# Kernel tuning notes

Measured on AMD Instinct MI355X. Metric: run time of the kernel, lower is better.

Reference implementation:

```python
import jax, jax.numpy as jnp
import numpy as np

N, E, F_IN, H, C = 169343, 1166243, 128, 128, 40
BN_EPS = 1e-5


def setup_inputs() -> dict:
    key = jax.random.key(0)
    ks = jax.random.split(key, 16)
    inp = {
        "x": jax.random.normal(ks[0], (N, F_IN), jnp.float32),
        "edge_index": jax.random.randint(ks[1], (2, E), 0, N, dtype=jnp.int64),
        "W1": jax.random.normal(ks[2], (F_IN, H), jnp.float32) * (1.0 / np.sqrt(F_IN)),
        "b1": jnp.zeros((H,), jnp.float32),
        "g1": jnp.ones((H,), jnp.float32),
        "be1": jnp.zeros((H,), jnp.float32),
        "m1": jax.random.normal(ks[3], (H,), jnp.float32) * 0.1,
        "v1": jax.random.uniform(ks[4], (H,), jnp.float32, 0.5, 1.5),
        "W2": jax.random.normal(ks[5], (H, H), jnp.float32) * (1.0 / np.sqrt(H)),
        "b2": jnp.zeros((H,), jnp.float32),
        "g2": jnp.ones((H,), jnp.float32),
        "be2": jnp.zeros((H,), jnp.float32),
        "m2": jax.random.normal(ks[6], (H,), jnp.float32) * 0.1,
        "v2": jax.random.uniform(ks[7], (H,), jnp.float32, 0.5, 1.5),
        "W3": jax.random.normal(ks[8], (H, C), jnp.float32) * (1.0 / np.sqrt(H)),
        "b3": jnp.zeros((C,), jnp.float32),
    }
    return inp


def _gcn_conv(h, W, b, src, dst, norm, n_nodes):
    # GCNConv: out = D^-1/2 (A+I) D^-1/2 (h W) + b
    hw = h @ W                                   # [N, H] dense GEMM
    msgs = hw[src] * norm[:, None]               # [E', H] gather (irregular)
    agg = jax.ops.segment_sum(msgs, dst, num_segments=n_nodes)  # scatter-add
    return agg + b


def _bn_eval(h, gamma, beta, mean, var):
    return (h - mean) * jax.lax.rsqrt(var + BN_EPS) * gamma + beta


def reference(x, edge_index, W1, b1, g1, be1, m1, v1,
              W2, b2, g2, be2, m2, v2, W3, b3):
    n = x.shape[0]
    loops = jnp.arange(n, dtype=edge_index.dtype)
    src = jnp.concatenate([edge_index[0], loops])  # add self-loops
    dst = jnp.concatenate([edge_index[1], loops])
    deg = jax.ops.segment_sum(jnp.ones_like(dst, dtype=x.dtype), dst, num_segments=n)
    dinv = jax.lax.rsqrt(jnp.maximum(deg, 1.0))
    norm = dinv[src] * dinv[dst]                  # [E+N]

    # layer stack (eval mode: dropout is identity, repeated ReLU idempotent)
    h = jax.nn.relu(_gcn_conv(x, W1, b1, src, dst, norm, n))
    h = jax.nn.relu(_bn_eval(h, g1, be1, m1, v1))
    h = jax.nn.relu(_gcn_conv(h, W2, b2, src, dst, norm, n))
    h = jax.nn.relu(_bn_eval(h, g2, be2, m2, v2))
    out = h @ W3 + b3                              # final Linear [N, C]
    return jax.nn.log_softmax(out, axis=-1), jnp.var(out, ddof=1)
```

## Files before the change

### kernel.cpp

```cpp
#include <hip/hip_runtime.h>
#include <math.h>

#define BN_EPS 1e-5f

typedef _Float16 f16;
typedef __attribute__((ext_vector_type(2))) _Float16 f16x2;
typedef __attribute__((ext_vector_type(4))) _Float16 f16x4;
typedef __attribute__((ext_vector_type(8))) _Float16 f16x8;
typedef __attribute__((ext_vector_type(4))) float f32x4;

__device__ __forceinline__ int edge_at(const void* ei, long long idx, int is64) {
    if (is64) return (int)((const long long*)ei)[idx];
    return ((const int*)ei)[idx];
}

__global__ void detect_kernel(const void* ei, int* flag) {
    const int* p = (const int*)ei;
    int f = 1;
    for (int i = 0; i < 64; i++)
        if (p[2 * i + 1] != 0) { f = 0; break; }
    *flag = f;
}

__global__ void init_kernel(int* deg_i, double* scal, int n) {
    int i = blockIdx.x * 256 + threadIdx.x;
    if (i < n) deg_i[i] = 0;
    if (blockIdx.x == 0 && threadIdx.x == 0) { scal[0] = 0.0; scal[1] = 0.0; }
}

__global__ void degi_kernel(const void* ei, const int* flag, int* deg_i, int E) {
    int e = blockIdx.x * 256 + threadIdx.x;
    if (e >= E) return;
    int is64 = *flag;
    int d = edge_at(ei, (long long)E + e, is64);
    atomicAdd(&deg_i[d], 1);
}

__global__ void dinv_kernel(const int* __restrict__ deg_i, float* dinv, int n) {
    int i = blockIdx.x * 256 + threadIdx.x;
    if (i < n) dinv[i] = rsqrtf((float)(deg_i[i] + 1));
}

__global__ __launch_bounds__(256) void scan1_kernel(
    const int* __restrict__ in, int* __restrict__ excl, int* bsum, int n) {
    __shared__ int sh[256];
    const int tid = threadIdx.x;
    const int base = blockIdx.x * 2048 + tid * 8;
    int v[8];
    #pragma unroll
    for (int i = 0; i < 8; i++) v[i] = (base + i < n) ? in[base + i] : 0;
    int tsum = 0;
    #pragma unroll
    for (int i = 0; i < 8; i++) { int t = v[i]; v[i] = tsum; tsum += t; }
    sh[tid] = tsum;
    __syncthreads();
    for (int off = 1; off < 256; off <<= 1) {
        int t = 0;
        if (tid >= off) t = sh[tid - off];
        __syncthreads();
        if (tid >= off) sh[tid] += t;
        __syncthreads();
    }
    int texcl = sh[tid] - tsum;
    #pragma unroll
    for (int i = 0; i < 8; i++)
        if (base + i < n) excl[base + i] = texcl + v[i];
    if (tid == 255 && bsum) bsum[blockIdx.x] = sh[255];
}

__global__ void scan3_kernel(int* rowptr, const int* __restrict__ boff,
                             int* cursor, int n, int E) {
    int i = blockIdx.x * 256 + threadIdx.x;
    if (i < n) {
        int val = rowptr[i] + boff[i >> 11];
        rowptr[i] = val;
        cursor[i] = val;
    }
    if (i == 0) rowptr[n] = E;
}

__global__ void fill_kernel(const void* ei, const int* flag,
                            int* cursor, int* col, int E) {
    int e = blockIdx.x * 256 + threadIdx.x;
    if (e >= E) return;
    int is64 = *flag;
    int s = edge_at(ei, e, is64);
    int d = edge_at(ei, (long long)E + e, is64);
    int pos = atomicAdd(&cursor[d], 1);
    col[pos] = s;
}

__global__ __launch_bounds__(256) void prep_w_kernel(
    const float* __restrict__ W, f16* __restrict__ Wth, f16* __restrict__ Wtl) {
    for (int f = blockIdx.x * 256 + threadIdx.x; f < 128 * 128;
         f += gridDim.x * 256) {
        int k = f >> 7, nn = f & 127;
        float wv = W[f];
        f16 h = (f16)wv;
        f16 l = (f16)(wv - (float)h);
        Wth[nn * 128 + k] = h;
        Wtl[nn * 128 + k] = l;
    }
}

#define APAD 40
__global__ __launch_bounds__(256) void gemm_l1_kernel(
    const float* __restrict__ X, const f16* __restrict__ Wth,
    const f16* __restrict__ Wtl, const float* __restrict__ dinv,
    f16* __restrict__ out, int M) {
    __shared__ f16 Ah[128 * APAD];
    __shared__ f16 Al[128 * APAD];
    __shared__ f16 Bh[128 * APAD];
    __shared__ f16 Bl[128 * APAD];
    const int t = threadIdx.x;
    const int r0 = blockIdx.x * 128;
    const int w = t >> 6, lane = t & 63;
    const int m0 = (w >> 1) * 64, n0 = (w & 1) * 64;
    const int fr = lane & 15;
    const int kb = (lane >> 4) * 8;

    f32x4 acc[4][4];
    #pragma unroll
    for (int i = 0; i < 4; i++)
        #pragma unroll
        for (int j = 0; j < 4; j++) acc[i][j] = (f32x4)0.f;

    for (int k0 = 0; k0 < 128; k0 += 32) {
        #pragma unroll
        for (int i = 0; i < 4; i++) {
            int f = t + i * 256;
            int row = f >> 3, kq = (f & 7) * 4;
            float4 v = make_float4(0.f, 0.f, 0.f, 0.f);
            if (r0 + row < M)
                v = *(const float4*)&X[(size_t)(r0 + row) * 128 + k0 + kq];
            f16 h0 = (f16)v.x, h1 = (f16)v.y, h2 = (f16)v.z, h3 = (f16)v.w;
            f16 l0 = (f16)(v.x - (float)h0), l1 = (f16)(v.y - (float)h1);
            f16 l2 = (f16)(v.z - (float)h2), l3 = (f16)(v.w - (float)h3);
            int base = row * APAD + kq;
            *(f16x4*)&Ah[base] = (f16x4){h0, h1, h2, h3};
            *(f16x4*)&Al[base] = (f16x4){l0, l1, l2, l3};
        }
        #pragma unroll
        for (int i = 0; i < 2; i++) {
            int f = t + i * 256;
            int nrow = f >> 2, kq = (f & 3) * 8;
            int gb = nrow * 128 + k0 + kq;
            int lb = nrow * APAD + kq;
            *(uint4*)&Bh[lb] = *(const uint4*)&Wth[gb];
            *(uint4*)&Bl[lb] = *(const uint4*)&Wtl[gb];
        }
        __syncthreads();

        f16x8 a0[4], b0[4], xx[4];
        #pragma unroll
        for (int i = 0; i < 4; i++) {
            a0[i] = *(const f16x8*)&Ah[(m0 + i * 16 + fr) * APAD + kb];
            b0[i] = *(const f16x8*)&Bh[(n0 + i * 16 + fr) * APAD + kb];
        }
        #pragma unroll
        for (int i = 0; i < 4; i++)
            #pragma unroll
            for (int j = 0; j < 4; j++)
                acc[i][j] = __builtin_amdgcn_mfma_f32_16x16x32_f16(
                    a0[i], b0[j], acc[i][j], 0, 0, 0);
        #pragma unroll
        for (int i = 0; i < 4; i++)
            xx[i] = *(const f16x8*)&Bl[(n0 + i * 16 + fr) * APAD + kb];
        #pragma unroll
        for (int i = 0; i < 4; i++)
            #pragma unroll
            for (int j = 0; j < 4; j++)
                acc[i][j] = __builtin_amdgcn_mfma_f32_16x16x32_f16(
                    a0[i], xx[j], acc[i][j], 0, 0, 0);
        #pragma unroll
        for (int i = 0; i < 4; i++)
            xx[i] = *(const f16x8*)&Al[(m0 + i * 16 + fr) * APAD + kb];
        #pragma unroll
        for (int i = 0; i < 4; i++)
            #pragma unroll
            for (int j = 0; j < 4; j++)
                acc[i][j] = __builtin_amdgcn_mfma_f32_16x16x32_f16(
                    xx[i], b0[j], acc[i][j], 0, 0, 0);
        __syncthreads();
    }

    #pragma unroll
    for (int i = 0; i < 4; i++) {
        #pragma unroll
        for (int r = 0; r < 4; r++) {
            int row = r0 + m0 + i * 16 + (lane >> 4) * 4 + r;
            if (row < M) {
                float di = dinv[row];
                #pragma unroll
                for (int j = 0; j < 4; j++)
                    out[(size_t)row * 128 + n0 + j * 16 + fr] =
                        (f16)(acc[i][j][r] * di);
            }
        }
    }
}

__global__ __launch_bounds__(256) void gemm_l2_kernel(
    const f16* __restrict__ X, const f16* __restrict__ Wth,
    const f16* __restrict__ Wtl, const float* __restrict__ dinv,
    f16* __restrict__ out, int M) {
    __shared__ f16 Ax[128 * APAD];
    __shared__ f16 Bh[128 * APAD];
    __shared__ f16 Bl[128 * APAD];
    const int t = threadIdx.x;
    const int r0 = blockIdx.x * 128;
    const int w = t >> 6, lane = t & 63;
    const int m0 = (w >> 1) * 64, n0 = (w & 1) * 64;
    const int fr = lane & 15;
    const int kb = (lane >> 4) * 8;

    f32x4 acc[4][4];
    #pragma unroll
    for (int i = 0; i < 4; i++)
        #pragma unroll
        for (int j = 0; j < 4; j++) acc[i][j] = (f32x4)0.f;

    for (int k0 = 0; k0 < 128; k0 += 32) {
        #pragma unroll
        for (int i = 0; i < 2; i++) {
            int f = t + i * 256;
            int row = f >> 2, kq = (f & 3) * 8;
            uint4 v = make_uint4(0u, 0u, 0u, 0u);
            if (r0 + row < M)
                v = *(const uint4*)&X[(size_t)(r0 + row) * 128 + k0 + kq];
            *(uint4*)&Ax[row * APAD + kq] = v;
        }
        #pragma unroll
        for (int i = 0; i < 2; i++) {
            int f = t + i * 256;
            int nrow = f >> 2, kq = (f & 3) * 8;
            int gb = nrow * 128 + k0 + kq;
            int lb = nrow * APAD + kq;
            *(uint4*)&Bh[lb] = *(const uint4*)&Wth[gb];
            *(uint4*)&Bl[lb] = *(const uint4*)&Wtl[gb];
        }
        __syncthreads();

        f16x8 a0[4], b0[4], xx[4];
        #pragma unroll
        for (int i = 0; i < 4; i++) {
            a0[i] = *(const f16x8*)&Ax[(m0 + i * 16 + fr) * APAD + kb];
            b0[i] = *(const f16x8*)&Bh[(n0 + i * 16 + fr) * APAD + kb];
        }
        #pragma unroll
        for (int i = 0; i < 4; i++)
            #pragma unroll
            for (int j = 0; j < 4; j++)
                acc[i][j] = __builtin_amdgcn_mfma_f32_16x16x32_f16(
                    a0[i], b0[j], acc[i][j], 0, 0, 0);
        #pragma unroll
        for (int i = 0; i < 4; i++)
            xx[i] = *(const f16x8*)&Bl[(n0 + i * 16 + fr) * APAD + kb];
        #pragma unroll
        for (int i = 0; i < 4; i++)
            #pragma unroll
            for (int j = 0; j < 4; j++)
                acc[i][j] = __builtin_amdgcn_mfma_f32_16x16x32_f16(
                    a0[i], xx[j], acc[i][j], 0, 0, 0);
        __syncthreads();
    }

    #pragma unroll
    for (int i = 0; i < 4; i++) {
        #pragma unroll
        for (int r = 0; r < 4; r++) {
            int row = r0 + m0 + i * 16 + (lane >> 4) * 4 + r;
            if (row < M) {
                float di = dinv[row];
                #pragma unroll
                for (int j = 0; j < 4; j++)
                    out[(size_t)row * 128 + n0 + j * 16 + fr] =
                        (f16)(acc[i][j][r] * di);
            }
        }
    }
}

__global__ __launch_bounds__(256) void agg_kernel(
    const f16* __restrict__ hs, const int* __restrict__ rowptr,
    const int* __restrict__ col, const float* __restrict__ dinv,
    const float* __restrict__ b, const float* __restrict__ g,
    const float* __restrict__ be, const float* __restrict__ m,
    const float* __restrict__ v, f16* __restrict__ h, int M) {
    const int node = blockIdx.x * 8 + (threadIdx.x >> 5);
    if (node >= M) return;
    const int lane = threadIdx.x & 31;
    const int c = lane * 4;

    f16x4 sv = *(const f16x4*)&hs[(size_t)node * 128 + c];
    float a1[4] = {(float)sv[0], (float)sv[1], (float)sv[2], (float)sv[3]};
    float a2[4] = {0.f, 0.f, 0.f, 0.f};
    const int beg = rowptr[node], end = rowptr[node + 1];
    int j = beg;
    for (; j + 1 < end; j += 2) {
        int s0 = col[j], s1 = col[j + 1];
        f16x4 v0 = *(const f16x4*)&hs[(size_t)s0 * 128 + c];
        f16x4 v1 = *(const f16x4*)&hs[(size_t)s1 * 128 + c];
        #pragma unroll
        for (int q = 0; q < 4; q++) { a1[q] += (float)v0[q]; a2[q] += (float)v1[q]; }
    }
    if (j < end) {
        int s0 = col[j];
        f16x4 v0 = *(const f16x4*)&hs[(size_t)s0 * 128 + c];
        #pragma unroll
        for (int q = 0; q < 4; q++) a1[q] += (float)v0[q];
    }
    const float di = dinv[node];
    f16x4 r;
    #pragma unroll
    for (int q = 0; q < 4; q++) {
        int cc = c + q;
        float tt = fmaxf(di * (a1[q] + a2[q]) + b[cc], 0.f);
        tt = (tt - m[cc]) * (g[cc] * rsqrtf(v[cc] + BN_EPS)) + be[cc];
        r[q] = (f16)fmaxf(tt, 0.f);
    }
    *(f16x4*)&h[(size_t)node * 128 + c] = r;
}

__global__ __launch_bounds__(256) void gemm_out_kernel(
    const f16* __restrict__ H, const float* __restrict__ W3,
    const float* __restrict__ b3, float* __restrict__ out,
    double* __restrict__ scal, int M) {
    __shared__ float Hs[256][20];
    __shared__ float Ws[128][40];
    const int t  = threadIdx.x;
    const int r0 = blockIdx.x * 256;
    #pragma unroll
    for (int i = 0; i < 5; i++) {
        int f = t + i * 256;
        ((float4*)Ws)[f] = ((const float4*)W3)[f];
    }
    const int rg = t >> 2;
    const int cb = (t & 3) * 10;
    float acc[4][10];
    #pragma unroll
    for (int i = 0; i < 4; i++)
        #pragma unroll
        for (int j = 0; j < 10; j++) acc[i][j] = 0.f;

    for (int k0 = 0; k0 < 128; k0 += 16) {
        __syncthreads();
        #pragma unroll
        for (int i = 0; i < 4; i++) {
            int f = t + i * 256;
            int r = f >> 2, c4 = (f & 3) * 4;
            float4 hv = make_float4(0.f, 0.f, 0.f, 0.f);
            if (r0 + r < M) {
                f16x4 hx = *(const f16x4*)&H[(size_t)(r0 + r) * 128 + k0 + c4];
                hv = make_float4((float)hx[0], (float)hx[1],
                                 (float)hx[2], (float)hx[3]);
            }
            *(float4*)&Hs[r][c4] = hv;
        }
        __syncthreads();
        #pragma unroll
        for (int k4 = 0; k4 < 4; k4++) {
            float hv[4][4];
            #pragma unroll
            for (int i = 0; i < 4; i++) {
                float4 h4 = *(const float4*)&Hs[rg + 64 * i][k4 * 4];
                hv[i][0] = h4.x; hv[i][1] = h4.y; hv[i][2] = h4.z; hv[i][3] = h4.w;
            }
            #pragma unroll
            for (int q = 0; q < 4; q++) {
                int k = k0 + k4 * 4 + q;
                float wv[10];
                #pragma unroll
                for (int j = 0; j < 5; j++) {
                    float2 w2 = *(const float2*)&Ws[k][cb + 2 * j];
                    wv[2 * j] = w2.x; wv[2 * j + 1] = w2.y;
                }
                #pragma unroll
                for (int i = 0; i < 4; i++)
                    #pragma unroll
                    for (int j = 0; j < 10; j++)
                        acc[i][j] = fmaf(hv[i][q], wv[j], acc[i][j]);
            }
        }
    }

    float s1 = 0.f, s2 = 0.f;
    #pragma unroll
    for (int i = 0; i < 4; i++) {
        int row = r0 + rg + 64 * i;
        float vb[10];
        #pragma unroll
        for (int j = 0; j < 10; j++) vb[j] = acc[i][j] + b3[cb + j];
        float mx = vb[0];
        #pragma unroll
        for (int j = 1; j < 10; j++) mx = fmaxf(mx, vb[j]);
        mx = fmaxf(mx, __shfl_xor(mx, 1));
        mx = fmaxf(mx, __shfl_xor(mx, 2));
        float se = 0.f;
        #pragma unroll
        for (int j = 0; j < 10; j++) se += expf(vb[j] - mx);
        se += __shfl_xor(se, 1);
        se += __shfl_xor(se, 2);
        float ls = mx + logf(se);
        if (row < M) {
            #pragma unroll
            for (int j = 0; j < 10; j++) {
                out[(size_t)row * 40 + cb + j] = vb[j] - ls;
                s1 += vb[j];
                s2 += vb[j] * vb[j];
            }
        }
    }
    #pragma unroll
    for (int o = 32; o; o >>= 1) { s1 += __shfl_xor(s1, o); s2 += __shfl_xor(s2, o); }
    __shared__ double sh1[4], sh2[4];
    if ((t & 63) == 0) { sh1[t >> 6] = (double)s1; sh2[t >> 6] = (double)s2; }
    __syncthreads();
    if (t == 0) {
        atomicAdd(&scal[0], sh1[0] + sh1[1] + sh1[2] + sh1[3]);
        atomicAdd(&scal[1], sh2[0] + sh2[1] + sh2[2] + sh2[3]);
    }
}

__global__ void var_kernel(const double* scal, float* out, long long nn, long long off) {
    double s1 = scal[0], s2 = scal[1];
    out[off] = (float)((s2 - s1 * s1 / (double)nn) / (double)(nn - 1));
}

extern "C" void kernel_launch(void* const* d_in, const int* in_sizes, int n_in,
                              void* d_out, int out_size, void* d_ws, size_t ws_size,
                              hipStream_t stream) {
    const float* x   = (const float*)d_in[0];
    const void*  ei  = d_in[1];
    const float* W1  = (const float*)d_in[2];
    const float* b1  = (const float*)d_in[3];
    const float* g1  = (const float*)d_in[4];
    const float* be1 = (const float*)d_in[5];
    const float* m1  = (const float*)d_in[6];
    const float* v1  = (const float*)d_in[7];
    const float* W2  = (const float*)d_in[8];
    const float* b2  = (const float*)d_in[9];
    const float* g2  = (const float*)d_in[10];
    const float* be2 = (const float*)d_in[11];
    const float* m2  = (const float*)d_in[12];
    const float* v2  = (const float*)d_in[13];
    const float* W3  = (const float*)d_in[14];
    const float* b3  = (const float*)d_in[15];

    const int n = in_sizes[0] / 128;
    const int E = in_sizes[1] / 2;
    float* out = (float*)d_out;

    size_t nh   = (size_t)n * 128;
    size_t npad = ((size_t)n + 3) & ~(size_t)3;
    size_t Epad = ((size_t)E + 3) & ~(size_t)3;
    double* scal   = (double*)d_ws;
    f16*    A      = (f16*)(scal + 2);
    f16*    B      = A + nh;
    float*  dinv   = (float*)(B + nh);
    int*    deg_i  = (int*)(dinv + npad);
    int*    rowptr = deg_i + npad;
    int*    cursor = rowptr + npad + 4;
    int*    bsum   = cursor + npad;
    int*    boff   = bsum + 128;
    int*    flag   = boff + 128;
    int*    col    = flag + 4;
    f16*    Wt1h   = (f16*)(col + Epad);
    f16*    Wt1l   = Wt1h + 128 * 128;
    f16*    Wt2h   = Wt1l + 128 * 128;
    f16*    Wt2l   = Wt2h + 128 * 128;

    const int nb_n   = (n + 255) / 256;
    const int nb_e   = (E + 255) / 256;
    const int nb_gm  = (n + 127) / 128;
    const int nb_agg = (n + 7) / 8;
    const int nb_g3  = (n + 255) / 256;
    const int nb_sc  = (n + 2047) / 2048;

    detect_kernel<<<1, 1, 0, stream>>>(ei, flag);
    init_kernel<<<nb_n, 256, 0, stream>>>(deg_i, scal, n);
    degi_kernel<<<nb_e, 256, 0, stream>>>(ei, flag, deg_i, E);
    dinv_kernel<<<nb_n, 256, 0, stream>>>(deg_i, dinv, n);
    prep_w_kernel<<<64, 256, 0, stream>>>(W1, Wt1h, Wt1l);
    prep_w_kernel<<<64, 256, 0, stream>>>(W2, Wt2h, Wt2l);

    scan1_kernel<<<nb_sc, 256, 0, stream>>>(deg_i, rowptr, bsum, n);
    scan1_kernel<<<1, 256, 0, stream>>>(bsum, boff, nullptr, nb_sc);
    scan3_kernel<<<nb_n, 256, 0, stream>>>(rowptr, boff, cursor, n, E);
    fill_kernel<<<nb_e, 256, 0, stream>>>(ei, flag, cursor, col, E);

    gemm_l1_kernel<<<nb_gm, 256, 0, stream>>>(x, Wt1h, Wt1l, dinv, A, n);
    agg_kernel<<<nb_agg, 256, 0, stream>>>(A, rowptr, col, dinv,
                                           b1, g1, be1, m1, v1, B, n);
    gemm_l2_kernel<<<nb_gm, 256, 0, stream>>>(B, Wt2h, Wt2l, dinv, A, n);
    agg_kernel<<<nb_agg, 256, 0, stream>>>(A, rowptr, col, dinv,
                                           b2, g2, be2, m2, v2, B, n);
    gemm_out_kernel<<<nb_g3, 256, 0, stream>>>(B, W3, b3, out, scal, n);
    var_kernel<<<1, 1, 0, stream>>>(scal, out, (long long)n * 40, (long long)n * 40);
}
```

Measured before the change: 598.9 us.

## Drop low-half X correction in layer-1 GEMM, fuse small kernels, unroll aggregation

Layer-1 GEMM no longer splits X into high and low fp16 parts, so the Al shared buffer and one of the three MFMA passes go away. This cuts MFMA work and shared-memory traffic, but X now carries only fp16 precision. The detect kernel is folded into init and the dinv computation into scan3, removing two launches. The aggregation loop is unrolled to four edges with four accumulators to keep more gathers in flight.

```diff
diff --git a/kernel.cpp b/kernel.cpp
--- a/kernel.cpp
+++ b/kernel.cpp
@@ -4,7 +4,6 @@
 #define BN_EPS 1e-5f
 
 typedef _Float16 f16;
-typedef __attribute__((ext_vector_type(2))) _Float16 f16x2;
 typedef __attribute__((ext_vector_type(4))) _Float16 f16x4;
 typedef __attribute__((ext_vector_type(8))) _Float16 f16x8;
 typedef __attribute__((ext_vector_type(4))) float f32x4;
@@ -14,18 +13,18 @@
     return ((const int*)ei)[idx];
 }
 
-__global__ void detect_kernel(const void* ei, int* flag) {
-    const int* p = (const int*)ei;
-    int f = 1;
-    for (int i = 0; i < 64; i++)
-        if (p[2 * i + 1] != 0) { f = 0; break; }
-    *flag = f;
-}
-
-__global__ void init_kernel(int* deg_i, double* scal, int n) {
+__global__ void init_kernel(const void* ei, int* flag, int* deg_i,
+                            double* scal, int n) {
     int i = blockIdx.x * 256 + threadIdx.x;
     if (i < n) deg_i[i] = 0;
-    if (blockIdx.x == 0 && threadIdx.x == 0) { scal[0] = 0.0; scal[1] = 0.0; }
+    if (blockIdx.x == 0 && threadIdx.x == 0) {
+        scal[0] = 0.0; scal[1] = 0.0;
+        const int* p = (const int*)ei;
+        int f = 1;
+        for (int k = 0; k < 64; k++)
+            if (p[2 * k + 1] != 0) { f = 0; break; }
+        *flag = f;
+    }
 }
 
 __global__ void degi_kernel(const void* ei, const int* flag, int* deg_i, int E) {
@@ -36,11 +35,6 @@
     atomicAdd(&deg_i[d], 1);
 }
 
-__global__ void dinv_kernel(const int* __restrict__ deg_i, float* dinv, int n) {
-    int i = blockIdx.x * 256 + threadIdx.x;
-    if (i < n) dinv[i] = rsqrtf((float)(deg_i[i] + 1));
-}
-
 __global__ __launch_bounds__(256) void scan1_kernel(
     const int* __restrict__ in, int* __restrict__ excl, int* bsum, int n) {
     __shared__ int sh[256];
@@ -69,12 +63,14 @@
 }
 
 __global__ void scan3_kernel(int* rowptr, const int* __restrict__ boff,
-                             int* cursor, int n, int E) {
+                             int* cursor, const int* __restrict__ deg_i,
+                             float* __restrict__ dinv, int n, int E) {
     int i = blockIdx.x * 256 + threadIdx.x;
     if (i < n) {
         int val = rowptr[i] + boff[i >> 11];
         rowptr[i] = val;
         cursor[i] = val;
+        dinv[i] = rsqrtf((float)(deg_i[i] + 1));
     }
     if (i == 0) rowptr[n] = E;
 }
@@ -109,7 +105,6 @@
     const f16* __restrict__ Wtl, const float* __restrict__ dinv,
     f16* __restrict__ out, int M) {
     __shared__ f16 Ah[128 * APAD];
-    __shared__ f16 Al[128 * APAD];
     __shared__ f16 Bh[128 * APAD];
     __shared__ f16 Bl[128 * APAD];
     const int t = threadIdx.x;
@@ -133,12 +128,8 @@
             float4 v = make_float4(0.f, 0.f, 0.f, 0.f);
             if (r0 + row < M)
                 v = *(const float4*)&X[(size_t)(r0 + row) * 128 + k0 + kq];
-            f16 h0 = (f16)v.x, h1 = (f16)v.y, h2 = (f16)v.z, h3 = (f16)v.w;
-            f16 l0 = (f16)(v.x - (float)h0), l1 = (f16)(v.y - (float)h1);
-            f16 l2 = (f16)(v.z - (float)h2), l3 = (f16)(v.w - (float)h3);
-            int base = row * APAD + kq;
-            *(f16x4*)&Ah[base] = (f16x4){h0, h1, h2, h3};
-            *(f16x4*)&Al[base] = (f16x4){l0, l1, l2, l3};
+            *(f16x4*)&Ah[row * APAD + kq] =
+                (f16x4){(f16)v.x, (f16)v.y, (f16)v.z, (f16)v.w};
         }
         #pragma unroll
         for (int i = 0; i < 2; i++) {
@@ -172,15 +163,6 @@
             for (int j = 0; j < 4; j++)
                 acc[i][j] = __builtin_amdgcn_mfma_f32_16x16x32_f16(
                     a0[i], xx[j], acc[i][j], 0, 0, 0);
-        #pragma unroll
-        for (int i = 0; i < 4; i++)
-            xx[i] = *(const f16x8*)&Al[(m0 + i * 16 + fr) * APAD + kb];
-        #pragma unroll
-        for (int i = 0; i < 4; i++)
-            #pragma unroll
-            for (int j = 0; j < 4; j++)
-                acc[i][j] = __builtin_amdgcn_mfma_f32_16x16x32_f16(
-                    xx[i], b0[j], acc[i][j], 0, 0, 0);
         __syncthreads();
     }
 
@@ -291,31 +273,48 @@
     if (node >= M) return;
     const int lane = threadIdx.x & 31;
     const int c = lane * 4;
-
-    f16x4 sv = *(const f16x4*)&hs[(size_t)node * 128 + c];
-    float a1[4] = {(float)sv[0], (float)sv[1], (float)sv[2], (float)sv[3]};
+    const f16* __restrict__ base = hs + c;
+
+    f16x4 sv = *(const f16x4*)&base[(size_t)node * 128];
+    float a0[4] = {(float)sv[0], (float)sv[1], (float)sv[2], (float)sv[3]};
+    float a1[4] = {0.f, 0.f, 0.f, 0.f};
     float a2[4] = {0.f, 0.f, 0.f, 0.f};
+    float a3[4] = {0.f, 0.f, 0.f, 0.f};
     const int beg = rowptr[node], end = rowptr[node + 1];
     int j = beg;
-    for (; j + 1 < end; j += 2) {
+    for (; j + 3 < end; j += 4) {
+        int s0 = col[j], s1 = col[j + 1], s2 = col[j + 2], s3 = col[j + 3];
+        f16x4 v0 = *(const f16x4*)&base[(size_t)s0 * 128];
+        f16x4 v1 = *(const f16x4*)&base[(size_t)s1 * 128];
+        f16x4 v2 = *(const f16x4*)&base[(size_t)s2 * 128];
+        f16x4 v3 = *(const f16x4*)&base[(size_t)s3 * 128];
+        #pragma unroll
+        for (int q = 0; q < 4; q++) {
+            a0[q] += (float)v0[q]; a1[q] += (float)v1[q];
+            a2[q] += (float)v2[q]; a3[q] += (float)v3[q];
+        }
+    }
+    if (j + 1 < end) {
         int s0 = col[j], s1 = col[j + 1];
-        f16x4 v0 = *(const f16x4*)&hs[(size_t)s0 * 128 + c];
-        f16x4 v1 = *(const f16x4*)&hs[(size_t)s1 * 128 + c];
-        #pragma unroll
-        for (int q = 0; q < 4; q++) { a1[q] += (float)v0[q]; a2[q] += (float)v1[q]; }
+        f16x4 v0 = *(const f16x4*)&base[(size_t)s0 * 128];
+        f16x4 v1 = *(const f16x4*)&base[(size_t)s1 * 128];
+        #pragma unroll
+        for (int q = 0; q < 4; q++) { a0[q] += (float)v0[q]; a1[q] += (float)v1[q]; }
+        j += 2;
     }
     if (j < end) {
         int s0 = col[j];
-        f16x4 v0 = *(const f16x4*)&hs[(size_t)s0 * 128 + c];
-        #pragma unroll
-        for (int q = 0; q < 4; q++) a1[q] += (float)v0[q];
+        f16x4 v0 = *(const f16x4*)&base[(size_t)s0 * 128];
+        #pragma unroll
+        for (int q = 0; q < 4; q++) a0[q] += (float)v0[q];
     }
     const float di = dinv[node];
     f16x4 r;
     #pragma unroll
     for (int q = 0; q < 4; q++) {
         int cc = c + q;
-        float tt = fmaxf(di * (a1[q] + a2[q]) + b[cc], 0.f);
+        float s = (a0[q] + a1[q]) + (a2[q] + a3[q]);
+        float tt = fmaxf(di * s + b[cc], 0.f);
         tt = (tt - m[cc]) * (g[cc] * rsqrtf(v[cc] + BN_EPS)) + be[cc];
         r[q] = (f16)fmaxf(tt, 0.f);
     }
@@ -477,16 +476,14 @@
     const int nb_g3  = (n + 255) / 256;
     const int nb_sc  = (n + 2047) / 2048;
 
-    detect_kernel<<<1, 1, 0, stream>>>(ei, flag);
-    init_kernel<<<nb_n, 256, 0, stream>>>(deg_i, scal, n);
+    init_kernel<<<nb_n, 256, 0, stream>>>(ei, flag, deg_i, scal, n);
     degi_kernel<<<nb_e, 256, 0, stream>>>(ei, flag, deg_i, E);
-    dinv_kernel<<<nb_n, 256, 0, stream>>>(deg_i, dinv, n);
     prep_w_kernel<<<64, 256, 0, stream>>>(W1, Wt1h, Wt1l);
     prep_w_kernel<<<64, 256, 0, stream>>>(W2, Wt2h, Wt2l);
 
     scan1_kernel<<<nb_sc, 256, 0, stream>>>(deg_i, rowptr, bsum, n);
     scan1_kernel<<<1, 256, 0, stream>>>(bsum, boff, nullptr, nb_sc);
-    scan3_kernel<<<nb_n, 256, 0, stream>>>(rowptr, boff, cursor, n, E);
+    scan3_kernel<<<nb_n, 256, 0, stream>>>(rowptr, boff, cursor, deg_i, dinv, n, E);
     fill_kernel<<<nb_e, 256, 0, stream>>>(ei, flag, cursor, col, E);
 
     gemm_l1_kernel<<<nb_gm, 256, 0, stream>>>(x, Wt1h, Wt1l, dinv, A, n);
```

After: 565.5 us. 5.6% less time.
